# Kernel optimization log

Measured on AMD Instinct MI355X. Metric: run time of the kernel, lower is better.

The kernel has to match this reference:

```python
import jax, jax.numpy as jnp
import numpy as np

H = 16  # num_heads


def setup_inputs() -> dict:
    key = jax.random.key(0)
    ks = jax.random.split(key, 9)
    L, N, E, I = 2048, 2, 2048, 2048
    s = 0.02
    return {
        "query": jax.random.normal(ks[0], (L, N, E), jnp.float32),
        "q_proj": jax.random.normal(ks[1], (I, E), jnp.float32) * s,
        "q_bias": jax.random.normal(ks[2], (I,), jnp.float32) * s,
        "k_proj": jax.random.normal(ks[3], (I, E), jnp.float32) * s,
        "k_bias": jax.random.normal(ks[4], (I,), jnp.float32) * s,
        "v_proj": jax.random.normal(ks[5], (I, E), jnp.float32) * s,
        "v_bias": jax.random.normal(ks[6], (I,), jnp.float32) * s,
        "out_proj": jax.random.normal(ks[7], (E, I), jnp.float32) * s,
        "out_bias": jax.random.normal(ks[8], (E,), jnp.float32) * s,
    }


def reference(query, q_proj, q_bias, k_proj, k_bias, v_proj, v_bias, out_proj, out_bias):
    L, N, E = query.shape
    h = H
    d = q_proj.shape[0] // h
    scale = d ** (-0.5)

    def split_heads(x):
        # [L, N, h*d] -> [N, h, L, d]  (matches view(L, N*h, d).transpose(0,1))
        return x.reshape(L, N, h, d).transpose(1, 2, 0, 3)

    q = split_heads(query @ q_proj.T + q_bias) * scale
    k = split_heads(query @ k_proj.T + k_bias)
    v = split_heads(query @ v_proj.T + v_bias)

    scores = jnp.einsum('nhld,nhkd->nhlk', q, k)  # [N, h, L, L]
    causal = jnp.tril(jnp.ones((L, L), dtype=bool))
    scores = jnp.where(causal, scores, jnp.float32(-10000.0))
    attn = jax.nn.softmax(scores, axis=-1)
    # dropout_p = 0.0 -> identity
    ctx = jnp.einsum('nhlk,nhkd->nhld', attn, v)
    ctx = ctx.transpose(2, 0, 1, 3).reshape(L, N, h * d)  # [L, N, h*d]
    return ctx @ out_proj.T + out_bias  # [L, N, E]
```

## Files before the change

### kernel.cpp

```cpp
#include <hip/hip_runtime.h>
#include <stdint.h>

#define L_SEQ 2048
#define NB 2
#define EMB 2048
#define II 2048
#define NH 16
#define DH 128
#define MROWS (L_SEQ * NB)

typedef __attribute__((ext_vector_type(8))) short bf16x8;
typedef __attribute__((ext_vector_type(4))) float f32x4;
typedef unsigned short u16;
typedef unsigned int u32;

__device__ __forceinline__ u16 f2bf(float f) {
  u32 u = __builtin_bit_cast(u32, f);
  u = u + 0x7fffu + ((u >> 16) & 1u);
  return (u16)(u >> 16);
}
__device__ __forceinline__ u16 f2bf_trunc(float f) {
  return (u16)(__builtin_bit_cast(u32, f) >> 16);
}

__device__ __forceinline__ void gl_lds16(const void* g, const u16* l) {
  __builtin_amdgcn_global_load_lds(
      (const __attribute__((address_space(1))) void*)(uintptr_t)g,
      (__attribute__((address_space(3))) void*)(u32)(uintptr_t)l, 16, 0, 0);
}

__global__ __launch_bounds__(256) void cast_all(
    const float* __restrict__ q, const float* __restrict__ w0, const float* __restrict__ w1,
    const float* __restrict__ w2, const float* __restrict__ w3, u16* __restrict__ dq,
    u16* __restrict__ dw) {
  const int b = blockIdx.x, t = threadIdx.x;
  const float* src;
  u16* dst;
  int idx;
  if (b < 8192) {
    src = q; dst = dq; idx = b * 256 + t;
  } else {
    int u = b - 8192;
    int sel = u >> 12;
    src = (sel == 0) ? w0 : (sel == 1) ? w1 : (sel == 2) ? w2 : w3;
    dst = dw + (size_t)sel * II * EMB;
    idx = (u & 4095) * 256 + t;
  }
  float4 v = ((const float4*)src)[idx];
  ushort4 o;
  o.x = f2bf(v.x); o.y = f2bf(v.y); o.z = f2bf(v.z); o.w = f2bf(v.w);
  ((ushort4*)dst)[idx] = o;
}

__global__ __launch_bounds__(256) void transpose_v(const u16* __restrict__ V,
                                                   u16* __restrict__ Vt) {
  __shared__ u16 tile[128][72];
  const int lb = blockIdx.x * 64;
  const int h = blockIdx.y;
  const u16* src = V + (size_t)h * L_SEQ * DH;
  u16* dst = Vt + (size_t)h * DH * L_SEQ;
  const int t = threadIdx.x;
  {
    const int l = t & 63, d0 = (t >> 6) * 32;
#pragma unroll
    for (int c = 0; c < 4; c++) {
      uint4 u = *(const uint4*)(src + (size_t)(lb + l) * DH + d0 + c * 8);
      const u16* e = (const u16*)&u;
#pragma unroll
      for (int x = 0; x < 8; x++) tile[d0 + c * 8 + x][l] = e[x];
    }
  }
  __syncthreads();
  {
    const int d = t >> 1, lc = (t & 1) * 32;
#pragma unroll
    for (int c = 0; c < 4; c++) {
      uint4 u = *(const uint4*)&tile[d][lc + c * 8];
      *(uint4*)(dst + (size_t)d * L_SEQ + lb + lc + c * 8) = u;
    }
  }
}

#define BK2 64
#define NT2 (EMB / BK2)

__global__ __launch_bounds__(512, 2) void gemm_2p(
    const u16* __restrict__ A, const u16* __restrict__ B, const float* __restrict__ b0,
    const float* __restrict__ b1, const float* __restrict__ b2, u16* __restrict__ out_bf,
    float* __restrict__ out_f, float qscale, int mode) {
  __shared__ __align__(16) u16 a_sm[2][8192];
  __shared__ __align__(16) u16 b_sm[3][16384];
  const int t = threadIdx.x;
  const int lane = t & 63, wv = t >> 6;
  const int quad = lane >> 4, l15 = lane & 15, x7 = l15 & 7;
  const int wm2 = wv >> 2, wn4 = wv & 3;
  const int srow = lane >> 3;
  const int schunk = (lane & 7) ^ (lane >> 3);

  const int bid = blockIdx.x;
  const int cpx = gridDim.x >> 3;
  const int swz = (bid & 7) * cpx + (bid >> 3);
  const int byy = swz & 31;
  const int bxx = swz >> 5;
  const int m0 = byy * 128, n0 = bxx * 256;

  const u16* abase = A + (size_t)m0 * EMB;
  const u16* bbase = B + (size_t)n0 * EMB;

  auto stageA = [&](int buf, int k0, int u) {
    int row = u * 64 + wv * 8 + srow;
    const u16* dst = (buf ? a_sm[1] : a_sm[0]) + u * 4096 + wv * 512;
    gl_lds16(abase + (size_t)row * EMB + k0 + schunk * 8, dst);
  };
  auto stageB = [&](int buf, int k0, int u) {
    int row = u * 64 + wv * 8 + srow;
    const u16* dst = (buf == 0 ? b_sm[0] : buf == 1 ? b_sm[1] : b_sm[2]) + u * 4096 + wv * 512;
    gl_lds16(bbase + (size_t)row * EMB + k0 + schunk * 8, dst);
  };

  stageB(0, 0, 0); stageB(0, 0, 1); stageB(0, 0, 2); stageB(0, 0, 3);
  stageA(0, 0, 0); stageA(0, 0, 1);
  stageB(1, BK2, 0); stageB(1, BK2, 1); stageB(1, BK2, 2); stageB(1, BK2, 3);
  stageA(1, BK2, 0); stageA(1, BK2, 1);
  __asm__ volatile("s_waitcnt vmcnt(0)" ::: "memory");
  __builtin_amdgcn_s_barrier();

  f32x4 acc[4][4] = {};
  int tB = 0;

#pragma unroll 1
  for (int tt = 0; tt < NT2; ++tt) {
    const u16* aC = (tt & 1) ? a_sm[1] : a_sm[0];
    const u16* bC = (tB == 0) ? b_sm[0] : (tB == 1) ? b_sm[1] : b_sm[2];
    const int tB2 = (tB + 2 >= 3) ? tB - 1 : tB + 2;
    const int kk2 = (tt + 2) * BK2;
    const bool pf2 = (tt + 2 < NT2);

    bf16x8 afr[4][2];

    {
#pragma unroll
      for (int mi = 0; mi < 4; mi++)
#pragma unroll
        for (int ks = 0; ks < 2; ks++)
          afr[mi][ks] = *(const bf16x8*)(aC + wm2 * 4096 + (mi * 16 + l15) * 64 +
                                         ((ks * 4 + quad) ^ x7) * 8);
      bf16x8 bfr[2][2];
#pragma unroll
      for (int nj = 0; nj < 2; nj++)
#pragma unroll
        for (int ks = 0; ks < 2; ks++)
          bfr[nj][ks] = *(const bf16x8*)(bC + wn4 * 4096 + (nj * 16 + l15) * 64 +
                                         ((ks * 4 + quad) ^ x7) * 8);
      if (pf2) { stageB(tB2, kk2, 0); stageB(tB2, kk2, 1); stageB(tB2, kk2, 2); stageB(tB2, kk2, 3); }
      __builtin_amdgcn_s_barrier();
      __builtin_amdgcn_s_setprio(1);
#pragma unroll
      for (int ks = 0; ks < 2; ks++)
#pragma unroll
        for (int mi = 0; mi < 4; mi++)
#pragma unroll
          for (int nj = 0; nj < 2; nj++)
            acc[mi][nj] =
                __builtin_amdgcn_mfma_f32_16x16x32_bf16(afr[mi][ks], bfr[nj][ks], acc[mi][nj], 0, 0, 0);
      __builtin_amdgcn_s_setprio(0);
      __builtin_amdgcn_s_barrier();
    }

    {
      bf16x8 bfr[2][2];
#pragma unroll
      for (int nj = 0; nj < 2; nj++)
#pragma unroll
        for (int ks = 0; ks < 2; ks++)
          bfr[nj][ks] = *(const bf16x8*)(bC + wn4 * 4096 + ((nj + 2) * 16 + l15) * 64 +
                                         ((ks * 4 + quad) ^ x7) * 8);
      if (pf2) {
        stageA(tt & 1, kk2, 0); stageA(tt & 1, kk2, 1);
        __asm__ volatile("s_waitcnt vmcnt(6)" ::: "memory");
      } else if (tt == NT2 - 2) {
        __asm__ volatile("s_waitcnt vmcnt(0)" ::: "memory");
      }
      __builtin_amdgcn_s_barrier();
      __builtin_amdgcn_s_setprio(1);
#pragma unroll
      for (int ks = 0; ks < 2; ks++)
#pragma unroll
        for (int mi = 0; mi < 4; mi++)
#pragma unroll
          for (int nj = 0; nj < 2; nj++)
            acc[mi][nj + 2] =
                __builtin_amdgcn_mfma_f32_16x16x32_bf16(afr[mi][ks], bfr[nj][ks], acc[mi][nj + 2], 0, 0, 0);
      __builtin_amdgcn_s_setprio(0);
      __builtin_amdgcn_s_barrier();
    }

    tB = (tB + 1 == 3) ? 0 : tB + 1;
  }

  if (mode == 0) {
    const int mat = n0 >> 11;
    const float* bp = (mat == 0) ? b0 : (mat == 1) ? b1 : b2;
    const float sc2 = (mat == 0) ? qscale : 1.0f;
#pragma unroll
    for (int mi = 0; mi < 4; mi++) {
#pragma unroll
      for (int nj = 0; nj < 4; nj++) {
#pragma unroll
        for (int r = 0; r < 4; r++) {
          int row = m0 + wm2 * 64 + mi * 16 + quad * 4 + r;
          int col = n0 + wn4 * 64 + nj * 16 + l15;
          int cc = col & 2047;
          float v = (acc[mi][nj][r] + bp[cc]) * sc2;
          int l = row >> 1, nb = row & 1;
          int hh = cc >> 7, dd = cc & 127;
          out_bf[(size_t)mat * MROWS * II + ((size_t)(nb * NH + hh) * L_SEQ + l) * DH + dd] =
              f2bf(v);
        }
      }
    }
  } else {
#pragma unroll
    for (int mi = 0; mi < 4; mi++) {
#pragma unroll
      for (int nj = 0; nj < 4; nj++) {
#pragma unroll
        for (int r = 0; r < 4; r++) {
          int row = m0 + wm2 * 64 + mi * 16 + quad * 4 + r;
          int col = n0 + wn4 * 64 + nj * 16 + l15;
          out_f[(size_t)row * EMB + col] = acc[mi][nj][r] + b0[col];
        }
      }
    }
  }
}

__global__ __launch_bounds__(256, 2) void flash_attn(
    const u16* __restrict__ Qh, const u16* __restrict__ Kh, const u16* __restrict__ Vt,
    u16* __restrict__ ctx) {
  __shared__ __align__(16) u16 k_sm[2][64 * 128];
  __shared__ __align__(16) u16 v_sm[2][128 * 64];
  __shared__ __align__(16) u16 p_sm[4][32 * 64];
  const int bx = blockIdx.x;
  const int nh = ((bx & 7) << 2) | ((bx >> 3) & 3);
  const int g = (bx >> 5) & 7;
  const int qt = (bx < 256) ? (15 - g) : g;
  const int q0 = qt * 128;
  const int nK = 2 * (qt + 1);
  const int t = threadIdx.x;
  const int lane = t & 63, wv = t >> 6;
  const int quad = lane >> 4, l15 = lane & 15;
  const int x7 = l15 & 7;
  const size_t hq = (size_t)nh * L_SEQ * DH;
  const u16* qp = Qh + hq;
  const u16* kp = Kh + hq;
  const u16* vp = Vt + hq;
  const int n = nh >> 4, h = nh & 15;
  const int srow = lane >> 4;
  const int spos = lane & 15;
  const int vrow = lane >> 3;
  const int vpos = lane & 7;
  u16* pwb = p_sm[wv];

  auto stageKV = [&](int bb, int kb) {
#pragma unroll
    for (int i = 0; i < 4; i++) {
      int ci = wv * 4 + i;
      int krow = ci * 4 + srow;
      int gck = spos ^ (krow & 7);
      gl_lds16(kp + (size_t)(kb + krow) * DH + gck * 8,
               (bb ? k_sm[1] : k_sm[0]) + ci * 512);
      int drow = ci * 8 + vrow;
      int gcv = vpos ^ (drow & 7);
      gl_lds16(vp + (size_t)drow * L_SEQ + kb + gcv * 8,
               (bb ? v_sm[1] : v_sm[0]) + ci * 512);
    }
  };

  bf16x8 qf[2][4];
#pragma unroll
  for (int mi = 0; mi < 2; mi++)
#pragma unroll
    for (int ks = 0; ks < 4; ks++)
      qf[mi][ks] = *(const bf16x8*)(qp + (size_t)(q0 + wv * 32 + mi * 16 + l15) * DH +
                                    ks * 32 + quad * 8);

  f32x4 o_acc[2][8] = {};
  float l_part[2][4] = {};

  stageKV(0, 0);

#pragma unroll 1
  for (int jb = 0; jb < nK; jb++) {
    const int b = jb & 1;
    const u16* kbuf = b ? k_sm[1] : k_sm[0];
    const u16* vbuf = b ? v_sm[1] : v_sm[0];
    const int kb = jb * 64;

    __syncthreads();
    if (jb + 1 < nK) stageKV(b ^ 1, kb + 64);

    f32x4 s[2][4] = {};
    __builtin_amdgcn_s_setprio(1);
#pragma unroll
    for (int nt = 0; nt < 4; nt++) {
#pragma unroll
      for (int ks = 0; ks < 4; ks++) {
        bf16x8 kf = *(const bf16x8*)(kbuf + (nt * 16 + l15) * 128 + ((ks * 4 + quad) ^ x7) * 8);
#pragma unroll
        for (int mi = 0; mi < 2; mi++)
          s[mi][nt] = __builtin_amdgcn_mfma_f32_16x16x32_bf16(qf[mi][ks], kf, s[mi][nt], 0, 0, 0);
      }
    }
    __builtin_amdgcn_s_setprio(0);

    const bool diag = (jb >= nK - 2);
#pragma unroll
    for (int mi = 0; mi < 2; mi++) {
      const int rowg = q0 + wv * 32 + mi * 16 + quad * 4;
#pragma unroll
      for (int nt = 0; nt < 4; nt++) {
        const int colg = kb + nt * 16 + l15;
#pragma unroll
        for (int r = 0; r < 4; r++) {
          float p = __builtin_amdgcn_exp2f(s[mi][nt][r]);
          if (diag && colg > rowg + r) p = 0.f;
          l_part[mi][r] += p;
          int pr = mi * 16 + quad * 4 + r;
          int chunk = nt * 2 + (l15 >> 3);
          int pos = chunk ^ (pr & 7);
          pwb[pr * 64 + pos * 8 + (l15 & 7)] = f2bf_trunc(p);
        }
      }
    }
    __asm__ volatile("s_waitcnt lgkmcnt(0)" ::: "memory");
    __builtin_amdgcn_sched_barrier(0);

    bf16x8 pf[2][2];
#pragma unroll
    for (int mi = 0; mi < 2; mi++)
#pragma unroll
      for (int ks = 0; ks < 2; ks++)
        pf[mi][ks] = *(const bf16x8*)(pwb + (mi * 16 + l15) * 64 + ((ks * 4 + quad) ^ x7) * 8);
    __builtin_amdgcn_s_setprio(1);
#pragma unroll
    for (int nt = 0; nt < 8; nt++) {
#pragma unroll
      for (int ks = 0; ks < 2; ks++) {
        bf16x8 vf = *(const bf16x8*)(vbuf + (nt * 16 + l15) * 64 + ((ks * 4 + quad) ^ x7) * 8);
#pragma unroll
        for (int mi = 0; mi < 2; mi++)
          o_acc[mi][nt] =
              __builtin_amdgcn_mfma_f32_16x16x32_bf16(pf[mi][ks], vf, o_acc[mi][nt], 0, 0, 0);
      }
    }
    __builtin_amdgcn_s_setprio(0);
  }

#pragma unroll
  for (int mi = 0; mi < 2; mi++) {
#pragma unroll
    for (int r = 0; r < 4; r++) {
      float lv = l_part[mi][r];
#pragma unroll
      for (int off = 1; off < 16; off <<= 1) lv += __shfl_xor(lv, off, 64);
      float inv = 1.f / lv;
      const int lrow = q0 + wv * 32 + mi * 16 + quad * 4 + r;
#pragma unroll
      for (int nt = 0; nt < 8; nt++) {
        int dd = nt * 16 + l15;
        ctx[((size_t)lrow * NB + n) * EMB + h * DH + dd] = f2bf(o_acc[mi][nt][r] * inv);
      }
    }
  }
}

extern "C" void kernel_launch(void* const* d_in, const int* in_sizes, int n_in,
                              void* d_out, int out_size, void* d_ws, size_t ws_size,
                              hipStream_t stream) {
  const float* query    = (const float*)d_in[0];
  const float* q_proj   = (const float*)d_in[1];
  const float* q_bias   = (const float*)d_in[2];
  const float* k_proj   = (const float*)d_in[3];
  const float* k_bias   = (const float*)d_in[4];
  const float* v_proj   = (const float*)d_in[5];
  const float* v_bias   = (const float*)d_in[6];
  const float* out_proj = (const float*)d_in[7];
  const float* out_bias = (const float*)d_in[8];

  u16* ws  = (u16*)d_ws;
  u16* Xbf = ws;
  u16* Wq  = Xbf + (size_t)MROWS * EMB;
  u16* Wk  = Wq + (size_t)II * EMB;
  u16* Wv  = Wk + (size_t)II * EMB;
  u16* Wo  = Wv + (size_t)II * EMB;
  u16* Qw  = Wo + (size_t)EMB * II;
  u16* Kw  = Qw + (size_t)MROWS * II;
  u16* Vw  = Kw + (size_t)MROWS * II;
  u16* Cw  = Vw + (size_t)MROWS * II;
  u16* Vtb = Xbf;

  cast_all<<<8192 + 4 * 4096, 256, 0, stream>>>(query, q_proj, k_proj, v_proj, out_proj,
                                                Xbf, Wq);

  const float qscale = 0.08838834764831845f * 1.4426950408889634f;
  gemm_2p<<<768, 512, 0, stream>>>(Xbf, Wq, q_bias, k_bias, v_bias, Qw, nullptr, qscale, 0);

  transpose_v<<<dim3(L_SEQ / 64, NB * NH), 256, 0, stream>>>(Vw, Vtb);

  flash_attn<<<512, 256, 0, stream>>>(Qw, Kw, Vtb, Cw);

  gemm_2p<<<256, 512, 0, stream>>>(Cw, Wo, out_bias, nullptr, nullptr, nullptr,
                                   (float*)d_out, 1.0f, 1);
}
```

Measured before the change: 369.8 us.

## Double-buffer LDS fragments in registers to overlap next-tile reads with MFMA

Restructures the projection GEMM main loop so each iteration loads the next K-tile's A and B fragments from LDS into a second register set while issuing MFMAs on the current set. The two half-steps per tile become one full step, and the loop is unrolled by two with ping-pong register buffers. This cuts the number of barriers per tile and hides LDS read latency behind matrix math. In exchange it doubles fragment register use, which may reduce occupancy. It also assumes NT2 is even and that the new waitcnt placement stays correct.

```diff
diff --git a/kernel.cpp b/kernel.cpp
--- a/kernel.cpp
+++ b/kernel.cpp
@@ -126,77 +126,66 @@
   __builtin_amdgcn_s_barrier();
 
   f32x4 acc[4][4] = {};
-  int tB = 0;
+  bf16x8 afr0[4][2], bfr0[4][2], afr1[4][2], bfr1[4][2];
+
+#pragma unroll
+  for (int mi = 0; mi < 4; mi++)
+#pragma unroll
+    for (int ks = 0; ks < 2; ks++)
+      afr0[mi][ks] = *(const bf16x8*)(a_sm[0] + wm2 * 4096 + (mi * 16 + l15) * 64 +
+                                      ((ks * 4 + quad) ^ x7) * 8);
+#pragma unroll
+  for (int nj = 0; nj < 4; nj++)
+#pragma unroll
+    for (int ks = 0; ks < 2; ks++)
+      bfr0[nj][ks] = *(const bf16x8*)(b_sm[0] + wn4 * 4096 + (nj * 16 + l15) * 64 +
+                                      ((ks * 4 + quad) ^ x7) * 8);
+  __asm__ volatile("s_waitcnt lgkmcnt(0)" ::: "memory");
+
+#define GBODY(TT, AFRU, BFRU, AFRL, BFRL)                                               \
+  {                                                                                     \
+    __builtin_amdgcn_s_barrier();               \
+    const int t2_ = (TT) + 2;                                                           \
+    if (t2_ < NT2) {                                                                    \
+      const int kk2_ = t2_ * BK2;                                                       \
+      const int bb2_ = t2_ % 3;                                                         \
+      stageB(bb2_, kk2_, 0); stageB(bb2_, kk2_, 1);                                     \
+      stageB(bb2_, kk2_, 2); stageB(bb2_, kk2_, 3);                                     \
+      stageA((TT) & 1, kk2_, 0); stageA((TT) & 1, kk2_, 1);                             \
+      __asm__ volatile("s_waitcnt vmcnt(6)" ::: "memory");                              \
+    } else if ((TT) + 1 < NT2) {                                                        \
+      __asm__ volatile("s_waitcnt vmcnt(0)" ::: "memory");                              \
+    }                                                                                   \
+    __builtin_amdgcn_s_barrier();             \
+    if ((TT) + 1 < NT2) {                                                               \
+      const u16* aN_ = (((TT) + 1) & 1) ? a_sm[1] : a_sm[0];                            \
+      const int bn1_ = ((TT) + 1) % 3;                                                  \
+      const u16* bN_ = bn1_ == 0 ? b_sm[0] : bn1_ == 1 ? b_sm[1] : b_sm[2];             \
+      _Pragma("unroll") for (int mi = 0; mi < 4; mi++)                                  \
+        _Pragma("unroll") for (int ks = 0; ks < 2; ks++)                                \
+          AFRL[mi][ks] = *(const bf16x8*)(aN_ + wm2 * 4096 + (mi * 16 + l15) * 64 +     \
+                                          ((ks * 4 + quad) ^ x7) * 8);                  \
+      _Pragma("unroll") for (int nj = 0; nj < 4; nj++)                                  \
+        _Pragma("unroll") for (int ks = 0; ks < 2; ks++)                                \
+          BFRL[nj][ks] = *(const bf16x8*)(bN_ + wn4 * 4096 + (nj * 16 + l15) * 64 +     \
+                                          ((ks * 4 + quad) ^ x7) * 8);                  \
+    }                                                                                   \
+    __builtin_amdgcn_s_setprio(1);                                                      \
+    _Pragma("unroll") for (int ks = 0; ks < 2; ks++)                                    \
+      _Pragma("unroll") for (int mi = 0; mi < 4; mi++)                                  \
+        _Pragma("unroll") for (int nj = 0; nj < 4; nj++)                                \
+          acc[mi][nj] = __builtin_amdgcn_mfma_f32_16x16x32_bf16(AFRU[mi][ks],           \
+                            BFRU[nj][ks], acc[mi][nj], 0, 0, 0);                        \
+    __builtin_amdgcn_s_setprio(0);                                                      \
+    __asm__ volatile("s_waitcnt lgkmcnt(0)" ::: "memory");                              \
+  }
 
 #pragma unroll 1
-  for (int tt = 0; tt < NT2; ++tt) {
-    const u16* aC = (tt & 1) ? a_sm[1] : a_sm[0];
-    const u16* bC = (tB == 0) ? b_sm[0] : (tB == 1) ? b_sm[1] : b_sm[2];
-    const int tB2 = (tB + 2 >= 3) ? tB - 1 : tB + 2;
-    const int kk2 = (tt + 2) * BK2;
-    const bool pf2 = (tt + 2 < NT2);
-
-    bf16x8 afr[4][2];
-
-    {
-#pragma unroll
-      for (int mi = 0; mi < 4; mi++)
-#pragma unroll
-        for (int ks = 0; ks < 2; ks++)
-          afr[mi][ks] = *(const bf16x8*)(aC + wm2 * 4096 + (mi * 16 + l15) * 64 +
-                                         ((ks * 4 + quad) ^ x7) * 8);
-      bf16x8 bfr[2][2];
-#pragma unroll
-      for (int nj = 0; nj < 2; nj++)
-#pragma unroll
-        for (int ks = 0; ks < 2; ks++)
-          bfr[nj][ks] = *(const bf16x8*)(bC + wn4 * 4096 + (nj * 16 + l15) * 64 +
-                                         ((ks * 4 + quad) ^ x7) * 8);
-      if (pf2) { stageB(tB2, kk2, 0); stageB(tB2, kk2, 1); stageB(tB2, kk2, 2); stageB(tB2, kk2, 3); }
-      __builtin_amdgcn_s_barrier();
-      __builtin_amdgcn_s_setprio(1);
-#pragma unroll
-      for (int ks = 0; ks < 2; ks++)
-#pragma unroll
-        for (int mi = 0; mi < 4; mi++)
-#pragma unroll
-          for (int nj = 0; nj < 2; nj++)
-            acc[mi][nj] =
-                __builtin_amdgcn_mfma_f32_16x16x32_bf16(afr[mi][ks], bfr[nj][ks], acc[mi][nj], 0, 0, 0);
-      __builtin_amdgcn_s_setprio(0);
-      __builtin_amdgcn_s_barrier();
-    }
-
-    {
-      bf16x8 bfr[2][2];
-#pragma unroll
-      for (int nj = 0; nj < 2; nj++)
-#pragma unroll
-        for (int ks = 0; ks < 2; ks++)
-          bfr[nj][ks] = *(const bf16x8*)(bC + wn4 * 4096 + ((nj + 2) * 16 + l15) * 64 +
-                                         ((ks * 4 + quad) ^ x7) * 8);
-      if (pf2) {
-        stageA(tt & 1, kk2, 0); stageA(tt & 1, kk2, 1);
-        __asm__ volatile("s_waitcnt vmcnt(6)" ::: "memory");
-      } else if (tt == NT2 - 2) {
-        __asm__ volatile("s_waitcnt vmcnt(0)" ::: "memory");
-      }
-      __builtin_amdgcn_s_barrier();
-      __builtin_amdgcn_s_setprio(1);
-#pragma unroll
-      for (int ks = 0; ks < 2; ks++)
-#pragma unroll
-        for (int mi = 0; mi < 4; mi++)
-#pragma unroll
-          for (int nj = 0; nj < 2; nj++)
-            acc[mi][nj + 2] =
-                __builtin_amdgcn_mfma_f32_16x16x32_bf16(afr[mi][ks], bfr[nj][ks], acc[mi][nj + 2], 0, 0, 0);
-      __builtin_amdgcn_s_setprio(0);
-      __builtin_amdgcn_s_barrier();
-    }
-
-    tB = (tB + 1 == 3) ? 0 : tB + 1;
-  }
+  for (int tt = 0; tt < NT2; tt += 2) {
+    GBODY(tt, afr0, bfr0, afr1, bfr1);
+    GBODY(tt + 1, afr1, bfr1, afr0, bfr0);
+  }
+#undef GBODY
 
   if (mode == 0) {
     const int mat = n0 >> 11;
```

New measurement: 399.3 us. 1.08x slower.

## Fuse V transpose into flash attention via register-staged LDS writes

Applied to the files above, without the earlier changes.

Removes the separate transpose_v kernel. Flash attention now loads V tiles in row-major form into registers and writes them to LDS transposed and swizzled, so the separate transpose pass, its launch and its global write and re-read of V go away. In exchange each iteration adds a full vmcnt(0) wait before the V write. That wait also covers the K async loads and may reduce load/compute overlap, and the staging buffer costs extra registers, which can affect the two-blocks-per-SIMD occupancy target.

```diff
diff --git a/kernel.cpp b/kernel.cpp
--- a/kernel.cpp
+++ b/kernel.cpp
@@ -52,35 +52,6 @@
   ((ushort4*)dst)[idx] = o;
 }
 
-__global__ __launch_bounds__(256) void transpose_v(const u16* __restrict__ V,
-                                                   u16* __restrict__ Vt) {
-  __shared__ u16 tile[128][72];
-  const int lb = blockIdx.x * 64;
-  const int h = blockIdx.y;
-  const u16* src = V + (size_t)h * L_SEQ * DH;
-  u16* dst = Vt + (size_t)h * DH * L_SEQ;
-  const int t = threadIdx.x;
-  {
-    const int l = t & 63, d0 = (t >> 6) * 32;
-#pragma unroll
-    for (int c = 0; c < 4; c++) {
-      uint4 u = *(const uint4*)(src + (size_t)(lb + l) * DH + d0 + c * 8);
-      const u16* e = (const u16*)&u;
-#pragma unroll
-      for (int x = 0; x < 8; x++) tile[d0 + c * 8 + x][l] = e[x];
-    }
-  }
-  __syncthreads();
-  {
-    const int d = t >> 1, lc = (t & 1) * 32;
-#pragma unroll
-    for (int c = 0; c < 4; c++) {
-      uint4 u = *(const uint4*)&tile[d][lc + c * 8];
-      *(uint4*)(dst + (size_t)d * L_SEQ + lb + lc + c * 8) = u;
-    }
-  }
-}
-
 #define BK2 64
 #define NT2 (EMB / BK2)
 
@@ -236,7 +207,7 @@
 }
 
 __global__ __launch_bounds__(256, 2) void flash_attn(
-    const u16* __restrict__ Qh, const u16* __restrict__ Kh, const u16* __restrict__ Vt,
+    const u16* __restrict__ Qh, const u16* __restrict__ Kh, const u16* __restrict__ Vr,
     u16* __restrict__ ctx) {
   __shared__ __align__(16) u16 k_sm[2][64 * 128];
   __shared__ __align__(16) u16 v_sm[2][128 * 64];
@@ -254,15 +225,17 @@
   const size_t hq = (size_t)nh * L_SEQ * DH;
   const u16* qp = Qh + hq;
   const u16* kp = Kh + hq;
-  const u16* vp = Vt + hq;
+  const u16* vsrc = Vr + hq;
   const int n = nh >> 4, h = nh & 15;
   const int srow = lane >> 4;
   const int spos = lane & 15;
-  const int vrow = lane >> 3;
-  const int vpos = lane & 7;
+  const int vkq = t >> 5;
+  const int vj = t & 31;
   u16* pwb = p_sm[wv];
 
-  auto stageKV = [&](int bb, int kb) {
+  uint2 vld[8];
+
+  auto stage_loads = [&](int bb, int kb) {
 #pragma unroll
     for (int i = 0; i < 4; i++) {
       int ci = wv * 4 + i;
@@ -270,10 +243,23 @@
       int gck = spos ^ (krow & 7);
       gl_lds16(kp + (size_t)(kb + krow) * DH + gck * 8,
                (bb ? k_sm[1] : k_sm[0]) + ci * 512);
-      int drow = ci * 8 + vrow;
-      int gcv = vpos ^ (drow & 7);
-      gl_lds16(vp + (size_t)drow * L_SEQ + kb + gcv * 8,
-               (bb ? v_sm[1] : v_sm[0]) + ci * 512);
+    }
+#pragma unroll
+    for (int i = 0; i < 8; i++)
+      vld[i] = *(const uint2*)(vsrc + (size_t)(kb + 8 * vkq + i) * DH + 4 * vj);
+  };
+  auto write_v = [&](int bb) {
+    u16* vb = bb ? v_sm[1] : v_sm[0];
+#pragma unroll
+    for (int r = 0; r < 4; r++) {
+      int row = 4 * vj + r;
+      int pos = vkq ^ (row & 7);
+      u32 w0 = (u32)((const u16*)&vld[0])[r] | ((u32)((const u16*)&vld[1])[r] << 16);
+      u32 w1 = (u32)((const u16*)&vld[2])[r] | ((u32)((const u16*)&vld[3])[r] << 16);
+      u32 w2 = (u32)((const u16*)&vld[4])[r] | ((u32)((const u16*)&vld[5])[r] << 16);
+      u32 w3 = (u32)((const u16*)&vld[6])[r] | ((u32)((const u16*)&vld[7])[r] << 16);
+      uint4 pk; pk.x = w0; pk.y = w1; pk.z = w2; pk.w = w3;
+      *(uint4*)(vb + row * 64 + pos * 8) = pk;
     }
   };
 
@@ -288,7 +274,9 @@
   f32x4 o_acc[2][8] = {};
   float l_part[2][4] = {};
 
-  stageKV(0, 0);
+  stage_loads(0, 0);
+  __asm__ volatile("s_waitcnt vmcnt(0)" ::: "memory");
+  write_v(0);
 
 #pragma unroll 1
   for (int jb = 0; jb < nK; jb++) {
@@ -298,7 +286,7 @@
     const int kb = jb * 64;
 
     __syncthreads();
-    if (jb + 1 < nK) stageKV(b ^ 1, kb + 64);
+    if (jb + 1 < nK) stage_loads(b ^ 1, kb + 64);
 
     f32x4 s[2][4] = {};
     __builtin_amdgcn_s_setprio(1);
@@ -355,6 +343,11 @@
       }
     }
     __builtin_amdgcn_s_setprio(0);
+
+    if (jb + 1 < nK) {
+      __asm__ volatile("s_waitcnt vmcnt(0)" ::: "memory");
+      write_v(b ^ 1);
+    }
   }
 
 #pragma unroll
@@ -398,7 +391,6 @@
   u16* Kw  = Qw + (size_t)MROWS * II;
   u16* Vw  = Kw + (size_t)MROWS * II;
   u16* Cw  = Vw + (size_t)MROWS * II;
-  u16* Vtb = Xbf;
 
   cast_all<<<8192 + 4 * 4096, 256, 0, stream>>>(query, q_proj, k_proj, v_proj, out_proj,
                                                 Xbf, Wq);
@@ -406,9 +398,7 @@
   const float qscale = 0.08838834764831845f * 1.4426950408889634f;
   gemm_2p<<<768, 512, 0, stream>>>(Xbf, Wq, q_bias, k_bias, v_bias, Qw, nullptr, qscale, 0);
 
-  transpose_v<<<dim3(L_SEQ / 64, NB * NH), 256, 0, stream>>>(Vw, Vtb);
-
-  flash_attn<<<512, 256, 0, stream>>>(Qw, Kw, Vtb, Cw);
+  flash_attn<<<512, 256, 0, stream>>>(Qw, Kw, Vw, Cw);
 
   gemm_2p<<<256, 512, 0, stream>>>(Cw, Wo, out_bias, nullptr, nullptr, nullptr,
                                    (float*)d_out, 1.0f, 1);
```

After: 367.6 us. No clear change (-0.6%).
